# Kernel tuning notes

Measured on AMD Instinct MI355X. Metric: run time of the kernel, lower is better.

Reference implementation:

```python
import jax, jax.numpy as jnp
import numpy as np

N = 50000
F_IN = 512
H1 = 500
H2 = 100
C = 16
E = 800000


def setup_inputs() -> dict:
    key = jax.random.key(0)
    ks = jax.random.split(key, 8)
    x = jax.random.normal(ks[0], (N, F_IN), dtype=jnp.float32)
    edge_index = jax.random.randint(ks[1], (2, E), 0, N, dtype=jnp.int64)
    W1 = jax.random.normal(ks[2], (F_IN, H1), dtype=jnp.float32) / np.sqrt(F_IN)
    b1 = jnp.zeros((H1,), dtype=jnp.float32)
    W2 = jax.random.normal(ks[3], (H1, H2), dtype=jnp.float32) / np.sqrt(H1)
    b2 = jnp.zeros((H2,), dtype=jnp.float32)
    W3 = jax.random.normal(ks[4], (H2, C), dtype=jnp.float32) / np.sqrt(H2)
    b3 = jnp.zeros((C,), dtype=jnp.float32)
    return {"x": x, "edge_index": edge_index, "W1": W1, "b1": b1,
            "W2": W2, "b2": b2, "W3": W3, "b3": b3}


def _edge_norm(edge_index, num_nodes):
    # add self loops (as in torch add_self_loops), then symmetric degree norm
    loops = jnp.arange(num_nodes, dtype=edge_index.dtype)
    row = jnp.concatenate([edge_index[0], loops])
    col = jnp.concatenate([edge_index[1], loops])
    deg = jax.ops.segment_sum(jnp.ones_like(row, dtype=jnp.float32), row,
                              num_segments=num_nodes)
    dinv = jnp.where(deg > 0, deg ** -0.5, 0.0)  # norm[isinf] = 0
    norm = dinv[row] * dinv[col]
    return row, col, norm


def _graph_conv(x, row, col, norm, W, b, num_nodes):
    h = x @ W + b                                  # [N, out]
    msg = norm[:, None] * h[col]                   # gather + scale, [E', out]
    return jax.ops.segment_sum(msg, row, num_segments=num_nodes)  # SpMM


def reference(x, edge_index, W1, b1, W2, b2, W3, b3):
    num_nodes = x.shape[0]
    row, col, norm = _edge_norm(edge_index, num_nodes)
    h = jnp.tanh(_graph_conv(x, row, col, norm, W1, b1, num_nodes))
    h = jnp.tanh(_graph_conv(h, row, col, norm, W2, b2, num_nodes))
    h = jnp.tanh(_graph_conv(h, row, col, norm, W3, b3, num_nodes))
    return jax.nn.softmax(h, axis=1)
```

## Files before the change

### kernel.cpp

```cpp
#include <hip/hip_runtime.h>
#include <math.h>

#define NN  50000
#define FIN 512
#define HH1 500
#define HH2 100
#define NC  16
#define NE  800000
#define KD  512

typedef __attribute__((ext_vector_type(4))) float    f32x4;
typedef __attribute__((ext_vector_type(4))) _Float16 f16x4;
typedef __attribute__((ext_vector_type(8))) _Float16 f16x8;
typedef __attribute__((ext_vector_type(8))) unsigned short u16x8;
typedef __attribute__((ext_vector_type(4))) unsigned short u16x4;


__global__ void zero2_k(int* a, int* b) {
    int i = blockIdx.x * blockDim.x + threadIdx.x;
    if (i < NN) { a[i] = 0; b[i] = 0; }
}

__global__ void hist_k(const int* __restrict__ rows, int* __restrict__ rowcnt) {
    int i = blockIdx.x * blockDim.x + threadIdx.x;
    if (i < NE) atomicAdd(&rowcnt[rows[i]], 1);
}

__global__ void dinv_k(const int* __restrict__ rowcnt, float* __restrict__ dinv) {
    int i = blockIdx.x * blockDim.x + threadIdx.x;
    if (i < NN) dinv[i] = rsqrtf((float)(rowcnt[i] + 1));
}

__global__ __launch_bounds__(1024) void scan1_k(const int* __restrict__ cnt,
                                                int* __restrict__ excl,
                                                int* __restrict__ bsum) {
    __shared__ int s[1024];
    int t = threadIdx.x;
    int i = blockIdx.x * 1024 + t;
    int v = (i < NN) ? cnt[i] : 0;
    s[t] = v;
    __syncthreads();
    #pragma unroll
    for (int off = 1; off < 1024; off <<= 1) {
        int add = (t >= off) ? s[t - off] : 0;
        __syncthreads();
        s[t] += add;
        __syncthreads();
    }
    if (i < NN) excl[i] = s[t] - v;
    if (t == 1023) bsum[blockIdx.x] = s[1023];
}

__global__ void scan2_k(int* bsum, int nb) {
    int lane = threadIdx.x;
    int orig = (lane < nb) ? bsum[lane] : 0;
    int v = orig;
    #pragma unroll
    for (int off = 1; off < 64; off <<= 1) {
        int u = __shfl_up(v, off, 64);
        if (lane >= off) v += u;
    }
    if (lane < nb) bsum[lane] = v - orig;
}

__global__ void scan3_k(const int* __restrict__ excl, const int* __restrict__ bsum,
                        int* __restrict__ ptr) {
    int i = blockIdx.x * 256 + threadIdx.x;
    if (i < NN) ptr[i] = excl[i] + bsum[i >> 10];
}

__global__ void scatter_k(const int* __restrict__ rows, const int* __restrict__ cols,
                          const float* __restrict__ dinv,
                          const int* __restrict__ row_ptr, int* __restrict__ fill,
                          int2* __restrict__ cw) {
    int e = blockIdx.x * blockDim.x + threadIdx.x;
    if (e >= NE) return;
    int r = rows[e], c = cols[e];
    int pos = row_ptr[r] + atomicAdd(&fill[r], 1);
    cw[pos] = make_int2(c, __float_as_int(dinv[r] * dinv[c]));
}


#define R1 (512 * 512)
#define R2 (128 * 512)
#define R3 (128 * 128)

__global__ void wconv3_k(const float* __restrict__ W1, const float* __restrict__ W2,
                         const float* __restrict__ W3, _Float16* __restrict__ Wt1,
                         _Float16* __restrict__ Wt2, _Float16* __restrict__ Wt3)
{
    int idx = blockIdx.x * 256 + threadIdx.x;
    if (idx < R1) {
        int n_ = idx >> 9, kk = idx & 511;
        float v = (n_ < HH1) ? W1[(size_t)kk * HH1 + n_] : 0.0f;
        Wt1[idx] = (_Float16)v;
    } else if (idx < R1 + R2) {
        int j = idx - R1;
        int n_ = j >> 9, kk = j & 511;
        float v = (kk < HH1 && n_ < HH2) ? W2[(size_t)kk * HH2 + n_] : 0.0f;
        Wt2[j] = (_Float16)v;
    } else if (idx < R1 + R2 + R3) {
        int j = idx - R1 - R2;
        int n_ = j >> 7, kk = j & 127;
        float v = (kk < HH2 && n_ < NC) ? W3[(size_t)kk * NC + n_] : 0.0f;
        Wt3[j] = (_Float16)v;
    }
}


typedef unsigned int u32g;

__device__ __forceinline__ void g2l16(const void* g, void* l) {
    __builtin_amdgcn_global_load_lds(
        (const __attribute__((address_space(1))) u32g*)g,
        (__attribute__((address_space(3))) u32g*)l, 16, 0, 0);
}


__global__ __launch_bounds__(256, 4) void gemm1_k(
    const float* __restrict__ A, const _Float16* __restrict__ Wt,
    const float* __restrict__ bias, _Float16* __restrict__ Cb, int n)
{
    __shared__ __align__(16) _Float16 As[2][64 * 32];
    __shared__ __align__(16) _Float16 Bs[2][256 * 32];

    int tid  = threadIdx.x;
    int lane = tid & 63;
    int w    = tid >> 6;
    int lr = lane & 15, q = lane >> 4;
    int row0 = blockIdx.x * 64;
    int col0 = blockIdx.y * 256;

    f32x4 acc[4][4];
    #pragma unroll
    for (int i = 0; i < 4; i++)
        #pragma unroll
        for (int j = 0; j < 4; j++) acc[i][j] = (f32x4){0.f, 0.f, 0.f, 0.f};

    int arr = tid >> 2, ac8 = tid & 3;
    int ac8s = ac8 ^ ((arr >> 1) & 3);
    int gr = row0 + arr; if (gr >= n) gr = n - 1;
    const float* asrc = A + (size_t)gr * 512 + ac8s * 8;

    float4 pav[2][2];

    auto aload = [&](int kt, int par) {
        pav[par][0] = *(const float4*)(asrc + kt);
        pav[par][1] = *(const float4*)(asrc + kt + 4);
    };
    auto astore = [&](int bf, int par) {
        float4 v0 = pav[par][0], v1 = pav[par][1];
        f16x8 h = {(_Float16)v0.x, (_Float16)v0.y, (_Float16)v0.z, (_Float16)v0.w,
                   (_Float16)v1.x, (_Float16)v1.y, (_Float16)v1.z, (_Float16)v1.w};
        *(f16x8*)&As[bf][tid * 8] = h;
    };
    auto bstage = [&](int kt, int bf) {
        #pragma unroll
        for (int i = 0; i < 4; i++) {
            int id = i * 256 + tid;
            int rr = id >> 2, c8 = id & 3;
            int c8s = c8 ^ ((rr >> 1) & 3);
            g2l16(Wt + (size_t)(col0 + rr) * 512 + kt + c8s * 8, &Bs[bf][id * 8]);
        }
    };

    aload(0, 0);
    aload(32, 1);
    bstage(0, 0);
    astore(0, 0);

    #pragma unroll
    for (int step = 0; step < 16; step++) {
        int bf = step & 1;
        __syncthreads();
        if (step + 2 < 16) aload((step + 2) * 32, bf);
        if (step + 1 < 16) bstage((step + 1) * 32, bf ^ 1);

        f16x8 a[4], b[4];
        #pragma unroll
        for (int t = 0; t < 4; t++) {
            int row = t * 16 + lr;
            a[t] = *(const f16x8*)&As[bf][(row * 4 + (q ^ ((row >> 1) & 3))) * 8];
        }
        #pragma unroll
        for (int t = 0; t < 4; t++) {
            int row = w * 64 + t * 16 + lr;
            b[t] = *(const f16x8*)&Bs[bf][(row * 4 + (q ^ ((row >> 1) & 3))) * 8];
        }
        #pragma unroll
        for (int ti = 0; ti < 4; ti++)
            #pragma unroll
            for (int tj = 0; tj < 4; tj++)
                acc[ti][tj] = __builtin_amdgcn_mfma_f32_16x16x32_f16(
                    a[ti], b[tj], acc[ti][tj], 0, 0, 0);

        if (step + 1 < 16) astore(bf ^ 1, bf ^ 1);
    }

    #pragma unroll
    for (int ti = 0; ti < 4; ti++) {
        #pragma unroll
        for (int tj = 0; tj < 4; tj++) {
            int col = col0 + w * 64 + tj * 16 + lr;
            bool valid = col < HH1;
            float bv = valid ? bias[col] : 0.0f;
            size_t cbase = (size_t)(col >> 8) * ((size_t)NN * 256) + (col & 255);
            #pragma unroll
            for (int p = 0; p < 4; p++) {
                int row = row0 + ti * 16 + q * 4 + p;
                if (row < n) {
                    float v = valid ? (acc[ti][tj][p] + bv) : 0.0f;
                    Cb[cbase + (size_t)row * 256] = (_Float16)v;
                }
            }
        }
    }
}


template<int BCOLS, int COUT, int KK>
__global__ __launch_bounds__(256, 3) void gemm_lds_k(
    const _Float16* __restrict__ A,
    const _Float16* __restrict__ Wt,
    const float* __restrict__ bias, _Float16* __restrict__ Cb,
    int mpad, int n, int m)
{
    constexpr int NBF   = BCOLS / 64;
    constexpr int WC    = BCOLS / 4;
    constexpr int NSTEP = KK / 32;

    __shared__ __align__(16) _Float16 As[2][64 * 32];
    __shared__ __align__(16) _Float16 Bs[2][BCOLS * 32];

    int tid  = threadIdx.x;
    int lane = tid & 63;
    int w    = tid >> 6;
    int lr = lane & 15, q = lane >> 4;
    int row0 = blockIdx.x * 64;
    int col0 = blockIdx.y * BCOLS;

    f32x4 acc[4][NBF];
    #pragma unroll
    for (int i = 0; i < 4; i++)
        #pragma unroll
        for (int j = 0; j < NBF; j++) acc[i][j] = (f32x4){0.f, 0.f, 0.f, 0.f};

    auto stage = [&](int kt, int bf) {
        {
            int rr = tid >> 2, c8 = tid & 3;
            int c8s = c8 ^ ((rr >> 1) & 3);
            int gr = row0 + rr; if (gr >= n) gr = n - 1;
            g2l16(A + (size_t)gr * KK + kt + c8s * 8, &As[bf][tid * 8]);
        }
        #pragma unroll
        for (int i = 0; i < NBF; i++) {
            int idx = i * 256 + tid;
            int rr = idx >> 2, c8 = idx & 3;
            int c8s = c8 ^ ((rr >> 1) & 3);
            g2l16(Wt + (size_t)(col0 + rr) * KK + kt + c8s * 8, &Bs[bf][idx * 8]);
        }
    };

    stage(0, 0);
    int bf = 0;
    #pragma unroll
    for (int step = 0; step < NSTEP; step++) {
        __syncthreads();
        if (step + 1 < NSTEP) stage((step + 1) * 32, bf ^ 1);

        f16x8 a[4], b[NBF];
        #pragma unroll
        for (int t = 0; t < 4; t++) {
            int row = t * 16 + lr;
            a[t] = *(const f16x8*)&As[bf][(row * 4 + (q ^ ((row >> 1) & 3))) * 8];
        }
        #pragma unroll
        for (int t = 0; t < NBF; t++) {
            int row = w * WC + t * 16 + lr;
            b[t] = *(const f16x8*)&Bs[bf][(row * 4 + (q ^ ((row >> 1) & 3))) * 8];
        }
        #pragma unroll
        for (int ti = 0; ti < 4; ti++)
            #pragma unroll
            for (int tj = 0; tj < NBF; tj++)
                acc[ti][tj] = __builtin_amdgcn_mfma_f32_16x16x32_f16(
                    a[ti], b[tj], acc[ti][tj], 0, 0, 0);
        bf ^= 1;
    }

    #pragma unroll
    for (int ti = 0; ti < 4; ti++) {
        #pragma unroll
        for (int tj = 0; tj < NBF; tj++) {
            int col = col0 + w * WC + tj * 16 + lr;
            if (COUT == 0 && col >= mpad) continue;
            bool valid = col < m;
            float bv = valid ? bias[col] : 0.0f;
            #pragma unroll
            for (int p = 0; p < 4; p++) {
                int row = row0 + ti * 16 + q * 4 + p;
                if (row < n) {
                    float v = valid ? (acc[ti][tj][p] + bv) : 0.0f;
                    if (COUT == 1) {
                        size_t addr = (size_t)(col >> 8) * ((size_t)NN * 256)
                                    + (size_t)row * 256 + (col & 255);
                        Cb[addr] = (_Float16)v;
                    } else {
                        Cb[(size_t)row * mpad + col] = (_Float16)v;
                    }
                }
            }
        }
    }
}


__device__ __forceinline__ void fma_mix8(float* acc, u16x8 v, float w) {
    union { u16x8 u; unsigned int d[4]; } t; t.u = v;
    #pragma unroll
    for (int k = 0; k < 4; k++) {
        asm("v_fma_mix_f32 %0, %1, %2, %0 op_sel:[0,0,0] op_sel_hi:[1,0,0]"
            : "+v"(acc[2 * k]) : "v"(t.d[k]), "v"(w));
        asm("v_fma_mix_f32 %0, %1, %2, %0 op_sel:[1,0,0] op_sel_hi:[1,0,0]"
            : "+v"(acc[2 * k + 1]) : "v"(t.d[k]), "v"(w));
    }
}

__device__ __forceinline__ void fma_mix4(float* acc, u16x4 v, float w) {
    union { u16x4 u; unsigned int d[2]; } t; t.u = v;
    #pragma unroll
    for (int k = 0; k < 2; k++) {
        asm("v_fma_mix_f32 %0, %1, %2, %0 op_sel:[0,0,0] op_sel_hi:[1,0,0]"
            : "+v"(acc[2 * k]) : "v"(t.d[k]), "v"(w));
        asm("v_fma_mix_f32 %0, %1, %2, %0 op_sel:[1,0,0] op_sel_hi:[1,0,0]"
            : "+v"(acc[2 * k + 1]) : "v"(t.d[k]), "v"(w));
    }
}


__global__ __launch_bounds__(256) void spmm_f16_256_k(
    const int* __restrict__ row_ptr, const int* __restrict__ rowcnt,
    const int2* __restrict__ cw, const float* __restrict__ dinv,
    const _Float16* __restrict__ hc,
    _Float16* __restrict__ outh, int fbase)
{
    int r = blockIdx.x * 4 + (threadIdx.x >> 6);
    int lane = threadIdx.x & 63;
    if (r >= NN) return;

    const u16x4* h4 = (const u16x4*)hc;

    float acc[4];
    #pragma unroll
    for (int i = 0; i < 4; i++) acc[i] = 0.f;

    float d = dinv[r];
    fma_mix4(acc, h4[(size_t)r * 64 + lane], d * d);

    int beg = row_ptr[r], cnt = rowcnt[r];
    for (int base = 0; base < cnt; base += 64) {
        int m = (cnt - base < 64) ? (cnt - base) : 64;
        int2 vc = (lane < m) ? cw[beg + base + lane] : make_int2(0, 0);
        int P = (m + 7) & ~7;
        for (int j = 0; j < P; j += 8) {
            u16x4 vv[8]; float wl[8];
            #pragma unroll
            for (int u = 0; u < 8; u++) {
                int c  = __builtin_amdgcn_readlane(vc.x, j + u);
                int wb = __builtin_amdgcn_readlane(vc.y, j + u);
                wl[u] = __int_as_float(wb);
                vv[u] = h4[(size_t)c * 64 + lane];
            }
            #pragma unroll
            for (int u = 0; u < 8; u++) fma_mix4(acc, vv[u], wl[u]);
        }
    }

    int f0 = fbase + lane * 4;
    f16x4 o;
    #pragma unroll
    for (int i = 0; i < 4; i++)
        o[i] = (_Float16)((f0 + i < HH1) ? tanhf(acc[i]) : 0.0f);
    __builtin_nontemporal_store(o, (f16x4*)(outh + (size_t)r * KD + f0));
}


__global__ __launch_bounds__(256) void spmm_f16_100_k(
    const int* __restrict__ row_ptr, const int* __restrict__ rowcnt,
    const int2* __restrict__ cw, const float* __restrict__ dinv,
    const _Float16* __restrict__ hb, _Float16* __restrict__ outh)
{
    int r = blockIdx.x * 16 + (threadIdx.x >> 4);
    int lane = threadIdx.x & 15;
    if (r >= NN) return;

    const u16x8* h8 = (const u16x8*)hb;

    float acc[8];
    #pragma unroll
    for (int i = 0; i < 8; i++) acc[i] = 0.f;

    float d = dinv[r];
    fma_mix8(acc, h8[(size_t)r * 16 + lane], d * d);

    int beg = row_ptr[r], cnt = rowcnt[r];
    int j = 0;
    for (; j + 7 < cnt; j += 8) {
        int2  e[8];
        u16x8 v[8];
        #pragma unroll
        for (int u = 0; u < 8; u++) e[u] = cw[beg + j + u];
        #pragma unroll
        for (int u = 0; u < 8; u++) v[u] = h8[(size_t)e[u].x * 16 + lane];
        #pragma unroll
        for (int u = 0; u < 8; u++) fma_mix8(acc, v[u], __int_as_float(e[u].y));
    }
    for (; j < cnt; j++) {
        int2 e = cw[beg + j];
        fma_mix8(acc, h8[(size_t)e.x * 16 + lane], __int_as_float(e.y));
    }

    int f0 = lane * 8;
    f16x8 o;
    #pragma unroll
    for (int i = 0; i < 8; i++)
        o[i] = (_Float16)((f0 + i < HH2) ? tanhf(acc[i]) : 0.0f);
    __builtin_nontemporal_store(o, (f16x8*)(outh + (size_t)r * 128 + f0));
}


__global__ __launch_bounds__(256) void spmm3h_k(
    const int* __restrict__ row_ptr, const int* __restrict__ rowcnt,
    const int2* __restrict__ cw, const float* __restrict__ dinv,
    const _Float16* __restrict__ hb, float* __restrict__ out)
{
    int r = blockIdx.x * 128 + (threadIdx.x >> 1);
    int lane = threadIdx.x & 1;
    if (r >= NN) return;

    const u16x8* h8 = (const u16x8*)hb;

    float acc[8];
    #pragma unroll
    for (int i = 0; i < 8; i++) acc[i] = 0.f;

    float d = dinv[r];
    fma_mix8(acc, h8[(size_t)r * 2 + lane], d * d);

    int beg = row_ptr[r], cnt = rowcnt[r];
    int j = 0;
    for (; j + 3 < cnt; j += 4) {
        int2  e0 = cw[beg + j],     e1 = cw[beg + j + 1];
        int2  e2 = cw[beg + j + 2], e3 = cw[beg + j + 3];
        u16x8 v0 = h8[(size_t)e0.x * 2 + lane];
        u16x8 v1 = h8[(size_t)e1.x * 2 + lane];
        u16x8 v2 = h8[(size_t)e2.x * 2 + lane];
        u16x8 v3 = h8[(size_t)e3.x * 2 + lane];
        fma_mix8(acc, v0, __int_as_float(e0.y));
        fma_mix8(acc, v1, __int_as_float(e1.y));
        fma_mix8(acc, v2, __int_as_float(e2.y));
        fma_mix8(acc, v3, __int_as_float(e3.y));
    }
    for (; j < cnt; j++) {
        int2 e = cw[beg + j];
        fma_mix8(acc, h8[(size_t)e.x * 2 + lane], __int_as_float(e.y));
    }

    float* o = out + (size_t)r * NC + lane * 8;
    f32x4 a0 = {acc[0], acc[1], acc[2], acc[3]};
    f32x4 a1 = {acc[4], acc[5], acc[6], acc[7]};
    __builtin_nontemporal_store(a0, (f32x4*)o);
    __builtin_nontemporal_store(a1, (f32x4*)(o + 4));
}

__global__ void tanh_softmax_k(const float* __restrict__ in, float* __restrict__ out) {
    int r = blockIdx.x * blockDim.x + threadIdx.x;
    if (r >= NN) return;
    float v[NC];
    float mx = -1e30f;
    #pragma unroll
    for (int j = 0; j < NC; j++) {
        v[j] = tanhf(in[r * NC + j]);
        mx = fmaxf(mx, v[j]);
    }
    float s = 0.0f;
    #pragma unroll
    for (int j = 0; j < NC; j++) { v[j] = expf(v[j] - mx); s += v[j]; }
    float inv = 1.0f / s;
    #pragma unroll
    for (int j = 0; j < NC; j++) out[r * NC + j] = v[j] * inv;
}


extern "C" void kernel_launch(void* const* d_in, const int* in_sizes, int n_in,
                              void* d_out, int out_size, void* d_ws, size_t ws_size,
                              hipStream_t stream)
{
    const float* x  = (const float*)d_in[0];
    const int*   ei = (const int*)d_in[1];
    const float* W1 = (const float*)d_in[2];
    const float* b1 = (const float*)d_in[3];
    const float* W2 = (const float*)d_in[4];
    const float* b2 = (const float*)d_in[5];
    const float* W3 = (const float*)d_in[6];
    const float* b3 = (const float*)d_in[7];
    float* out = (float*)d_out;

    const int* rows = ei;
    const int* cols = ei + NE;

    char* p = (char*)d_ws;
    float*     dinv    = (float*)p;     p += (size_t)NN * 4;
    int*       rowcnt  = (int*)p;       p += (size_t)NN * 4;
    int*       row_ptr = (int*)p;       p += (size_t)NN * 4;
    int*       fill    = (int*)p;       p += (size_t)NN * 4;
    int*       excl    = (int*)p;       p += (size_t)NN * 4;
    int*       bsum    = (int*)p;       p += (size_t)256 * 4;
    int2*      cw      = (int2*)p;      p += (size_t)NE * 8;
    float*     B3      = (float*)p;     p += (size_t)NN * NC * 4;
    _Float16*  A1h     = (_Float16*)p;  p += (size_t)NN * KD * 2;
    _Float16*  h1h     = (_Float16*)p;  p += (size_t)NN * KD * 2;
    _Float16*  A2h     = (_Float16*)p;  p += (size_t)NN * 128 * 2;
    _Float16*  h2h     = (_Float16*)p;  p += (size_t)NN * 128 * 2;
    _Float16*  A3h     = (_Float16*)p;  p += (size_t)NN * NC * 2;
    _Float16*  Wt1     = (_Float16*)p;  p += (size_t)R1 * 2;
    _Float16*  Wt2     = (_Float16*)p;  p += (size_t)R2 * 2;
    _Float16*  Wt3     = (_Float16*)p;  p += (size_t)R3 * 2;

    const int T = 256;
    const int NB = (NN + 1023) / 1024;
    const int GB = (NN + 63) / 64;

    wconv3_k<<<(R1 + R2 + R3) / 256, T, 0, stream>>>(W1, W2, W3, Wt1, Wt2, Wt3);
    zero2_k<<<(NN + T - 1) / T, T, 0, stream>>>(rowcnt, fill);
    hist_k<<<(NE + T - 1) / T, T, 0, stream>>>(rows, rowcnt);
    dinv_k<<<(NN + T - 1) / T, T, 0, stream>>>(rowcnt, dinv);
    scan1_k<<<NB, 1024, 0, stream>>>(rowcnt, excl, bsum);
    scan2_k<<<1, 64, 0, stream>>>(bsum, NB);
    scan3_k<<<(NN + T - 1) / T, T, 0, stream>>>(excl, bsum, row_ptr);
    scatter_k<<<(NE + T - 1) / T, T, 0, stream>>>(rows, cols, dinv, row_ptr, fill, cw);

    {
        gemm1_k<<<dim3(GB, 2), T, 0, stream>>>(x, Wt1, b1, A1h, NN);
        spmm_f16_256_k<<<(NN + 3) / 4, T, 0, stream>>>(row_ptr, rowcnt, cw, dinv,
                                                       A1h, h1h, 0);
        spmm_f16_256_k<<<(NN + 3) / 4, T, 0, stream>>>(row_ptr, rowcnt, cw, dinv,
                                                       A1h + (size_t)NN * 256, h1h, 256);
    }
    {
        gemm_lds_k<128, 0, 512><<<dim3(GB, 1), T, 0, stream>>>(
            h1h, Wt2, b2, A2h, 128, NN, HH2);
        spmm_f16_100_k<<<(NN + 15) / 16, T, 0, stream>>>(row_ptr, rowcnt, cw,
                                                         dinv, A2h, h2h);
    }
    {
        gemm_lds_k<64, 0, 128><<<dim3(GB, 1), T, 0, stream>>>(
            h2h, Wt3, b3, A3h, NC, NN, NC);
        spmm3h_k<<<(NN + 127) / 128, T, 0, stream>>>(row_ptr, rowcnt, cw,
                                                     dinv, A3h, B3);
        tanh_softmax_k<<<(NN + T - 1) / T, T, 0, stream>>>(B3, out);
    }
}
```

Before: 530.4 us.

## Deepen GEMM software pipelines with explicit vmcnt waits and triple buffering

Reworks the prefetch schedule in both GEMM kernels. The first-layer GEMM now loads A three K-steps ahead using inline-asm global loads and a 3-deep register buffer. The other GEMMs move to triple-buffered LDS with prefetch two steps ahead. Full __syncthreads are replaced by fine-grained s_waitcnt vmcnt/lgkmcnt plus a raw s_barrier, so loads can stay in flight across the MFMA phase. Launch-bound occupancy hints are also swapped. The cost is more registers and LDS, and a risk of correctness bugs if the hand-counted vmcnt values are wrong.

```diff
diff --git a/kernel.cpp b/kernel.cpp
--- a/kernel.cpp
+++ b/kernel.cpp
@@ -14,6 +14,14 @@
 typedef __attribute__((ext_vector_type(8))) _Float16 f16x8;
 typedef __attribute__((ext_vector_type(8))) unsigned short u16x8;
 typedef __attribute__((ext_vector_type(4))) unsigned short u16x4;
+
+template<int N>
+__device__ __forceinline__ void waitv() {
+    asm volatile("s_waitcnt vmcnt(%0)" :: "n"(N) : "memory");
+}
+__device__ __forceinline__ void waitlgkm0() {
+    asm volatile("s_waitcnt lgkmcnt(0)" ::: "memory");
+}
 
 
 __global__ void zero2_k(int* a, int* b) {
@@ -117,7 +125,7 @@
 }
 
 
-__global__ __launch_bounds__(256, 4) void gemm1_k(
+__global__ __launch_bounds__(256, 3) void gemm1_k(
     const float* __restrict__ A, const _Float16* __restrict__ Wt,
     const float* __restrict__ bias, _Float16* __restrict__ Cb, int n)
 {
@@ -142,16 +150,19 @@
     int gr = row0 + arr; if (gr >= n) gr = n - 1;
     const float* asrc = A + (size_t)gr * 512 + ac8s * 8;
 
-    float4 pav[2][2];
+    f32x4 pav[3][2];
 
     auto aload = [&](int kt, int par) {
-        pav[par][0] = *(const float4*)(asrc + kt);
-        pav[par][1] = *(const float4*)(asrc + kt + 4);
+        const float* p0 = asrc + kt;
+        asm volatile("global_load_dwordx4 %0, %2, off\n\t"
+                     "global_load_dwordx4 %1, %2, off offset:16"
+                     : "=&v"(pav[par][0]), "=&v"(pav[par][1])
+                     : "v"(p0) : "memory");
     };
     auto astore = [&](int bf, int par) {
-        float4 v0 = pav[par][0], v1 = pav[par][1];
-        f16x8 h = {(_Float16)v0.x, (_Float16)v0.y, (_Float16)v0.z, (_Float16)v0.w,
-                   (_Float16)v1.x, (_Float16)v1.y, (_Float16)v1.z, (_Float16)v1.w};
+        f32x4 v0 = pav[par][0], v1 = pav[par][1];
+        f16x8 h = {(_Float16)v0[0], (_Float16)v0[1], (_Float16)v0[2], (_Float16)v0[3],
+                   (_Float16)v1[0], (_Float16)v1[1], (_Float16)v1[2], (_Float16)v1[3]};
         *(f16x8*)&As[bf][tid * 8] = h;
     };
     auto bstage = [&](int kt, int bf) {
@@ -164,29 +175,33 @@
         }
     };
 
+    bstage(0, 0);
     aload(0, 0);
     aload(32, 1);
-    bstage(0, 0);
+    aload(64, 2);
+    waitv<4>();
+    __builtin_amdgcn_sched_barrier(0);
     astore(0, 0);
-
-    #pragma unroll
-    for (int step = 0; step < 16; step++) {
-        int bf = step & 1;
-        __syncthreads();
-        if (step + 2 < 16) aload((step + 2) * 32, bf);
-        if (step + 1 < 16) bstage((step + 1) * 32, bf ^ 1);
-
+    waitlgkm0();
+    __builtin_amdgcn_s_barrier();
+
+    #pragma unroll
+    for (int s = 0; s < 16; s++) {
         f16x8 a[4], b[4];
         #pragma unroll
         for (int t = 0; t < 4; t++) {
             int row = t * 16 + lr;
-            a[t] = *(const f16x8*)&As[bf][(row * 4 + (q ^ ((row >> 1) & 3))) * 8];
+            a[t] = *(const f16x8*)&As[s & 1][(row * 4 + (q ^ ((row >> 1) & 3))) * 8];
         }
         #pragma unroll
         for (int t = 0; t < 4; t++) {
             int row = w * 64 + t * 16 + lr;
-            b[t] = *(const f16x8*)&Bs[bf][(row * 4 + (q ^ ((row >> 1) & 3))) * 8];
-        }
+            b[t] = *(const f16x8*)&Bs[s & 1][(row * 4 + (q ^ ((row >> 1) & 3))) * 8];
+        }
+
+        if (s + 1 < 16) bstage((s + 1) * 32, (s + 1) & 1);
+        if (s + 3 < 16) aload((s + 3) * 32, (s + 3) % 3);
+
         #pragma unroll
         for (int ti = 0; ti < 4; ti++)
             #pragma unroll
@@ -194,7 +209,16 @@
                 acc[ti][tj] = __builtin_amdgcn_mfma_f32_16x16x32_f16(
                     a[ti], b[tj], acc[ti][tj], 0, 0, 0);
 
-        if (step + 1 < 16) astore(bf ^ 1, bf ^ 1);
+        if (s + 1 < 16) {
+            if (s <= 12)      waitv<12>();
+            else if (s == 13) waitv<10>();
+            else              waitv<8>();
+            __builtin_amdgcn_sched_barrier(0);
+            astore((s + 1) & 1, (s + 1) % 3);
+            if (s <= 12) waitv<2>(); else waitv<0>();
+            waitlgkm0();
+            __builtin_amdgcn_s_barrier();
+        }
     }
 
     #pragma unroll
@@ -219,7 +243,7 @@
 
 
 template<int BCOLS, int COUT, int KK>
-__global__ __launch_bounds__(256, 3) void gemm_lds_k(
+__global__ __launch_bounds__(256, 4) void gemm_lds_k(
     const _Float16* __restrict__ A,
     const _Float16* __restrict__ Wt,
     const float* __restrict__ bias, _Float16* __restrict__ Cb,
@@ -228,9 +252,10 @@
     constexpr int NBF   = BCOLS / 64;
     constexpr int WC    = BCOLS / 4;
     constexpr int NSTEP = KK / 32;
-
-    __shared__ __align__(16) _Float16 As[2][64 * 32];
-    __shared__ __align__(16) _Float16 Bs[2][BCOLS * 32];
+    constexpr int G     = 1 + NBF;
+
+    __shared__ __align__(16) _Float16 As[3][64 * 32];
+    __shared__ __align__(16) _Float16 Bs[3][BCOLS * 32];
 
     int tid  = threadIdx.x;
     int lane = tid & 63;
@@ -262,12 +287,13 @@
     };
 
     stage(0, 0);
-    int bf = 0;
-    #pragma unroll
-    for (int step = 0; step < NSTEP; step++) {
-        __syncthreads();
-        if (step + 1 < NSTEP) stage((step + 1) * 32, bf ^ 1);
-
+    stage(32, 1);
+    waitv<G>();
+    __builtin_amdgcn_s_barrier();
+
+    #pragma unroll
+    for (int s = 0; s < NSTEP; s++) {
+        int bf = s % 3;
         f16x8 a[4], b[NBF];
         #pragma unroll
         for (int t = 0; t < 4; t++) {
@@ -279,13 +305,20 @@
             int row = w * WC + t * 16 + lr;
             b[t] = *(const f16x8*)&Bs[bf][(row * 4 + (q ^ ((row >> 1) & 3))) * 8];
         }
+
+        if (s + 2 < NSTEP) stage((s + 2) * 32, (s + 2) % 3);
+
         #pragma unroll
         for (int ti = 0; ti < 4; ti++)
             #pragma unroll
             for (int tj = 0; tj < NBF; tj++)
                 acc[ti][tj] = __builtin_amdgcn_mfma_f32_16x16x32_f16(
                     a[ti], b[tj], acc[ti][tj], 0, 0, 0);
-        bf ^= 1;
+
+        if (s + 1 < NSTEP) {
+            if (s + 2 < NSTEP) waitv<G>(); else waitv<0>();
+            __builtin_amdgcn_s_barrier();
+        }
     }
 
     #pragma unroll
```

Measured after the change: 533.1 us. No clear change (+0.5%).
